# Performance work log

Measured on AMD Instinct MI355X. Metric: run time of the kernel, lower is better.

Reference implementation:

```python
import jax, jax.numpy as jnp
import numpy as np

H = 256   # hidden_dim
S = 16    # d_state
B = 2
N = 8192
LN_EPS = 1e-5


def setup_inputs() -> dict:
    key = jax.random.key(0)
    ks = jax.random.split(key, 12)
    std = 1.0 / np.sqrt(H)
    inp = {
        'x': jax.random.normal(ks[0], (B, N, H), dtype=jnp.float32),
        'in_w': jax.random.normal(ks[1], (2 * H, H), dtype=jnp.float32) * std,
        'in_b': jax.random.normal(ks[2], (2 * H,), dtype=jnp.float32) * std,
        'xp_w': jax.random.normal(ks[3], (2 * S + 1, H), dtype=jnp.float32) * std,
        'xp_b': jax.random.normal(ks[4], (2 * S + 1,), dtype=jnp.float32) * std,
        'dt_w': jax.random.normal(ks[5], (H, 1), dtype=jnp.float32),
        'dt_b': jax.random.normal(ks[6], (H,), dtype=jnp.float32),
        'A_log': jnp.log(jnp.broadcast_to(jnp.arange(1, S + 1, dtype=jnp.float32), (H, S))),
        'D': jnp.ones((H,), dtype=jnp.float32),
        'out_w': jax.random.normal(ks[7], (H, H), dtype=jnp.float32) * std,
        'out_b': jax.random.normal(ks[8], (H,), dtype=jnp.float32) * std,
        'ln_g': jnp.ones((H,), dtype=jnp.float32),
        'ln_b': jnp.zeros((H,), dtype=jnp.float32),
    }
    return inp


def reference(x, in_w, in_b, xp_w, xp_b, dt_w, dt_b, A_log, D, out_w, out_b, ln_g, ln_b):
    # x: (B, N, H). Dropout is identity in eval mode.
    residual = x
    xz = jnp.einsum('bnh,kh->bnk', x, in_w) + in_b            # (B,N,2H)
    x_inner, z = xz[..., :H], xz[..., H:]
    x_dbl = jnp.einsum('bnh,kh->bnk', x_inner, xp_w) + xp_b   # (B,N,2S+1)
    dt_raw = x_dbl[..., :1]
    B_raw = x_dbl[..., 1:S + 1]                               # (B,N,S)
    C_raw = x_dbl[..., S + 1:]                                # (B,N,S)
    dt = jax.nn.softplus(dt_raw * dt_w[:, 0] + dt_b)          # (B,N,H)
    # NOTE: the original computes dA = exp(dt * A) but never uses it; A_log
    # does not affect the output, so we skip materializing dA.
    dB = dt[..., None] * B_raw[:, :, None, :]                 # (B,N,H,S)
    h = jnp.cumsum(x_inner[..., None] * dB, axis=1)           # (B,N,H,S)
    y = jnp.einsum('bnhs,bns->bnh', h, C_raw) + D * x_inner   # (B,N,H)
    y = y * jax.nn.silu(z)
    out = jnp.einsum('bnh,kh->bnk', y, out_w) + out_b
    r = out + residual
    mu = jnp.mean(r, axis=-1, keepdims=True)
    var = jnp.mean((r - mu) ** 2, axis=-1, keepdims=True)
    return ln_g * (r - mu) * jax.lax.rsqrt(var + LN_EPS) + ln_b
```

## Files before the change

kernel.cpp:

```cpp
#include <hip/hip_runtime.h>
#include <hip/hip_bf16.h>


#define HD 256
#define SD 16
#define NSEQ 8192
#define NBATCH 2
#define BN (NBATCH * NSEQ)
#define CHUNK 32
#define NCHUNK (NSEQ / CHUNK)
#define NGRP 16
#define GSZ (NCHUNK / NGRP)
#define LN_EPS 1e-5f
#define UST 40
#define YST 257

#define NX  (BN * HD)
#define NIW (2 * HD * HD)
#define NXP (48 * HD)
#define NOW (HD * HD)

typedef __hip_bfloat16 bf16;
typedef __attribute__((ext_vector_type(8))) short bf16x8;
typedef __attribute__((ext_vector_type(4))) short short4v;
typedef __attribute__((ext_vector_type(4))) float f32x4;
typedef __attribute__((ext_vector_type(4))) unsigned int uint4v;
typedef __attribute__((ext_vector_type(2))) unsigned int uint2v;

__device__ __forceinline__ float b2f(bf16 v) { return __bfloat162float(v); }
__device__ __forceinline__ short f2bs(float f) {
  union { bf16 b; short s; } u;
  u.b = __float2bfloat16(f);
  return u.s;
}
__device__ __forceinline__ unsigned int pack2(float a, float b) {
  return (unsigned int)(unsigned short)f2bs(a) |
         ((unsigned int)(unsigned short)f2bs(b) << 16);
}
__device__ __forceinline__ bf16x8 cvt_frag(const float* p) {
  bf16x8 r;
#pragma unroll
  for (int j = 0; j < 8; ++j) r[j] = f2bs(p[j]);
  return r;
}
__device__ __forceinline__ float softplus_f(float a) {
  return (a > 20.f) ? a : __logf(1.f + __expf(a));
}

__global__ __launch_bounds__(256) void k0_convert(
    const float* __restrict__ x, const float* __restrict__ in_w,
    const float* __restrict__ xp_w, const float* __restrict__ out_w,
    bf16* __restrict__ xb, bf16* __restrict__ wbin,
    bf16* __restrict__ wbxp, bf16* __restrict__ wbout)
{
  const int base = (blockIdx.x * 256 + threadIdx.x) * 4;
  if (base < NX) {
    f32x4 v = *(const f32x4*)(x + base);
    *(short4v*)((short*)xb + base) =
        short4v{f2bs(v[0]), f2bs(v[1]), f2bs(v[2]), f2bs(v[3])};
  } else if (base < NX + NIW) {
    const int off = base - NX;
    f32x4 v = *(const f32x4*)(in_w + off);
    *(short4v*)((short*)wbin + off) =
        short4v{f2bs(v[0]), f2bs(v[1]), f2bs(v[2]), f2bs(v[3])};
  } else if (base < NX + NIW + NXP) {
    const int off = base - NX - NIW;
    short4v s;
    if (off < 33 * HD) {
      f32x4 v = *(const f32x4*)(xp_w + off);
      s = short4v{f2bs(v[0]), f2bs(v[1]), f2bs(v[2]), f2bs(v[3])};
    } else {
      s = short4v{0, 0, 0, 0};
    }
    *(short4v*)((short*)wbxp + off) = s;
  } else if (base < NX + NIW + NXP + NOW) {
    const int off = base - NX - NIW - NXP;
    f32x4 v = *(const f32x4*)(out_w + off);
    *(short4v*)((short*)wbout + off) =
        short4v{f2bs(v[0]), f2bs(v[1]), f2bs(v[2]), f2bs(v[3])};
  }
}

__global__ __launch_bounds__(256) void k1_gemm(
    const bf16* __restrict__ xb, const bf16* __restrict__ wbin,
    const float* __restrict__ in_b, bf16* __restrict__ xib,
    bf16* __restrict__ zb)
{
  __shared__ __align__(16) char smem[128 * 264 * 2];
  bf16* Bt = (bf16*)smem;
  float* Ct = (float*)smem;

  const int tid = threadIdx.x;
  const int rt = blockIdx.x >> 2, ct = blockIdx.x & 3;
  const int R0 = rt * 128, C0 = ct * 128;
  const int wave = tid >> 6, lane = tid & 63, q = lane >> 4, l16 = lane & 15;

#pragma unroll
  for (int it = 0; it < 16; ++it) {
    const int f = tid + it * 256;
    const int row = f >> 5, g = f & 31;
    bf16x8 v = *(const bf16x8*)(wbin + (size_t)(C0 + row) * HD + g * 8);
    *(bf16x8*)(Bt + row * 264 + g * 8) = v;
  }
  __syncthreads();

  const int rowHalf = (wave & 1) * 64;
  const int colHalf = (wave >> 1) * 64;
  f32x4 acc[4][4] = {};
  const bf16* ap = xb + (size_t)(R0 + rowHalf + l16) * HD + q * 8;
#pragma unroll
  for (int k = 0; k < HD; k += 32) {
    bf16x8 a[4], b[4];
#pragma unroll
    for (int i = 0; i < 4; ++i)
      a[i] = *(const bf16x8*)(ap + (size_t)i * 16 * HD + k);
#pragma unroll
    for (int j = 0; j < 4; ++j)
      b[j] = *(const bf16x8*)(Bt + (colHalf + j * 16 + l16) * 264 + k + q * 8);
#pragma unroll
    for (int i = 0; i < 4; ++i)
#pragma unroll
      for (int j = 0; j < 4; ++j)
        acc[i][j] = __builtin_amdgcn_mfma_f32_16x16x32_bf16(a[i], b[j], acc[i][j], 0, 0, 0);
  }
  __syncthreads();

#pragma unroll
  for (int j = 0; j < 4; ++j) {
    const int col = colHalf + j * 16 + l16;
    const float bias = in_b[C0 + col];
#pragma unroll
    for (int i = 0; i < 4; ++i)
#pragma unroll
      for (int r = 0; r < 4; ++r)
        Ct[(rowHalf + i * 16 + q * 4 + r) * 132 + col] = acc[i][j][r] + bias;
  }
  __syncthreads();

  bf16* dst = (C0 < HD) ? xib : zb;
  const int Cd = (C0 < HD) ? C0 : (C0 - HD);
#pragma unroll
  for (int it = 0; it < 8; ++it) {
    const int f = tid + it * 256;
    const int row = f >> 4, g = f & 15;
    bf16x8 v = cvt_frag(Ct + row * 132 + g * 8);
    *(bf16x8*)(dst + (size_t)(R0 + row) * HD + Cd + g * 8) = v;
  }
}

__global__ __launch_bounds__(256) void kS_xp_sum(
    const bf16* __restrict__ xib, const bf16* __restrict__ wbxp,
    const float* __restrict__ xp_b, const float* __restrict__ dt_w,
    const float* __restrict__ dt_b, float* __restrict__ dbc,
    bf16* __restrict__ Tg, float* __restrict__ Mc)
{
  __shared__ __align__(16) bf16 xt[32 * 264];
  __shared__ __align__(16) bf16 wp[48 * 264];
  __shared__ __align__(16) float sdbc[32][33];
  __shared__ __align__(16) bf16 sBt[16 * UST];
  __shared__ __align__(16) bf16 Ut[256 * UST];
  const int tid = threadIdx.x;
  const int wave = tid >> 6, lane = tid & 63, q = lane >> 4, l16 = lane & 15;
  const int cix = blockIdx.x;
  const int R0 = cix * CHUNK;

#pragma unroll
  for (int it = 0; it < 4; ++it) {
    const int f = tid + it * 256, row = f >> 5, g = f & 31;
    *(bf16x8*)(xt + row * 264 + g * 8) =
        *(const bf16x8*)(xib + (size_t)(R0 + row) * HD + g * 8);
  }
#pragma unroll
  for (int it = 0; it < 6; ++it) {
    const int f = tid + it * 256, row = f >> 5, g = f & 31;
    *(bf16x8*)(wp + row * 264 + g * 8) =
        *(const bf16x8*)(wbxp + (size_t)row * HD + g * 8);
  }
  __syncthreads();

  if (wave < 2) {
    f32x4 pacc[3] = {};
#pragma unroll
    for (int k = 0; k < HD; k += 32) {
      bf16x8 af = *(const bf16x8*)(xt + (wave * 16 + l16) * 264 + k + q * 8);
#pragma unroll
      for (int t = 0; t < 3; ++t) {
        bf16x8 bfr = *(const bf16x8*)(wp + (t * 16 + l16) * 264 + k + q * 8);
        pacc[t] = __builtin_amdgcn_mfma_f32_16x16x32_bf16(af, bfr, pacc[t], 0, 0, 0);
      }
    }
#pragma unroll
    for (int t = 0; t < 3; ++t) {
      const int col = t * 16 + l16;
      if (col < 33) {
        const float bias = xp_b[col];
#pragma unroll
        for (int r = 0; r < 4; ++r) {
          const int row = wave * 16 + q * 4 + r;
          const float v = pacc[t][r] + bias;
          sdbc[row][col] = v;
          if (col >= 1 && col < 17)
            *((short*)sBt + (col - 1) * UST + row) = f2bs(v);
        }
      }
    }
  }
  __syncthreads();

  {
    const float* sflat = &sdbc[0][0];
    for (int idx = tid; idx < CHUNK * 33; idx += 256)
      dbc[(size_t)R0 * 33 + idx] = sflat[idx];
  }
  {
    const int h = tid;
    const float dtw = dt_w[h], dtb = dt_b[h];
    unsigned int up[16];
#pragma unroll
    for (int n2 = 0; n2 < 16; ++n2) {
      const int n = 2 * n2;
      const float xv0 = b2f(xt[n * 264 + h]);
      const float xv1 = b2f(xt[(n + 1) * 264 + h]);
      const float u0 = xv0 * softplus_f(sdbc[n][0] * dtw + dtb);
      const float u1 = xv1 * softplus_f(sdbc[n + 1][0] * dtw + dtb);
      up[n2] = pack2(u0, u1);
    }
    uint4v* dst = (uint4v*)(Ut + h * UST);
#pragma unroll
    for (int j = 0; j < 4; ++j)
      dst[j] = uint4v{up[4 * j], up[4 * j + 1], up[4 * j + 2], up[4 * j + 3]};
  }
  {
    const int n = tid >> 3;
    const int m0 = (tid & 7) * 4;
    float cn[SD];
#pragma unroll
    for (int s = 0; s < SD; ++s) cn[s] = sdbc[n][17 + s];
    short4v tv;
#pragma unroll
    for (int mm = 0; mm < 4; ++mm) {
      const int m = m0 + mm;
      float t = 0.f;
#pragma unroll
      for (int s = 0; s < SD; ++s) t += cn[s] * sdbc[m][1 + s];
      tv[mm] = (m <= n) ? f2bs(t) : (short)0;
    }
    *(short4v*)((short*)Tg + (size_t)cix * 1024 + n * 32 + m0) = tv;
  }
  __syncthreads();

  {
    bf16x8 af = *(const bf16x8*)(sBt + l16 * UST + q * 8);
    f32x4 macc[4] = {};
#pragma unroll
    for (int c4 = 0; c4 < 4; ++c4) {
      const int ct = wave * 4 + c4;
      bf16x8 bu = *(const bf16x8*)(Ut + (ct * 16 + l16) * UST + q * 8);
      macc[c4] = __builtin_amdgcn_mfma_f32_16x16x32_bf16(af, bu, macc[c4], 0, 0, 0);
    }
    float* mbase = Mc + (size_t)cix * 4096;
#pragma unroll
    for (int c4 = 0; c4 < 4; ++c4) {
      const int h = (wave * 4 + c4) * 16 + l16;
#pragma unroll
      for (int r = 0; r < 4; ++r)
        mbase[(q * 4 + r) * HD + h] = macc[c4][r];
    }
  }
}

__global__ __launch_bounds__(256) void k4a_prefix_local(
    float* __restrict__ Mc, float* __restrict__ Gs)
{
  const int tid = blockIdx.x * 256 + threadIdx.x;
  const int b = tid >> 16;
  const int g = (tid >> 12) & (NGRP - 1);
  const int hs = tid & 4095;
  float run = 0.f;
#pragma unroll
  for (int i = 0; i < GSZ; ++i) {
    const size_t idx = ((size_t)(b * NCHUNK + g * GSZ + i)) * 4096 + hs;
    const float v = Mc[idx];
    Mc[idx] = run;
    run += v;
  }
  Gs[((size_t)(b * NGRP + g)) * 4096 + hs] = run;
}

__global__ __launch_bounds__(256) void k4b_prefix_groups(float* __restrict__ Gs)
{
  const int tid = blockIdx.x * 256 + threadIdx.x;
  const int b = tid >> 12;
  const int hs = tid & 4095;
  float run = 0.f;
#pragma unroll
  for (int g = 0; g < NGRP; ++g) {
    const size_t idx = ((size_t)(b * NGRP + g)) * 4096 + hs;
    const float v = Gs[idx];
    Gs[idx] = run;
    run += v;
  }
}

__global__ __launch_bounds__(256) void k56_scan_out_ln(
    const bf16* __restrict__ xib, const bf16* __restrict__ zb,
    const float* __restrict__ dbc, const bf16* __restrict__ Tg,
    const float* __restrict__ dt_w, const float* __restrict__ dt_b,
    const float* __restrict__ Dv, const float* __restrict__ Mc,
    const float* __restrict__ Gs, const bf16* __restrict__ wbout,
    const float* __restrict__ out_b, const float* __restrict__ x,
    const float* __restrict__ ln_g, const float* __restrict__ ln_b,
    float* __restrict__ out)
{
  __shared__ __align__(16) char un[2 * 32 * YST * 4];
  bf16* Ut  = (bf16*)un;
  bf16* Hst = (bf16*)(un + 20480);
  bf16* Ctl = (bf16*)(un + 40960);
  bf16* Tt  = (bf16*)(un + 43520);
  float* yt = (float*)un;
  float* pt = (float*)(un + 32 * YST * 4);
  __shared__ float sdt[32];

  const int tid = threadIdx.x;
  const int wave = tid >> 6, lane = tid & 63, q = lane >> 4, l16 = lane & 15;
  const int cix = blockIdx.x;
  const int R0 = cix * CHUNK;
  const int b = cix >> 8;
  const int cchunk = cix & 255;

  *(short4v*)((short*)Tt + tid * 4) =
      *(const short4v*)((const short*)Tg + (size_t)cix * 1024 + tid * 4);
  if (tid < 32) sdt[tid] = dbc[(size_t)(R0 + tid) * 33];
  {
    const int n = tid >> 3, k0 = (tid & 7) * 4;
    float v[4];
#pragma unroll
    for (int j = 0; j < 4; ++j) {
      const int k = k0 + j;
      v[j] = (k < SD) ? dbc[(size_t)(R0 + n) * 33 + 17 + k] : 0.f;
    }
    *(uint2v*)((short*)Ctl + n * UST + k0) = uint2v{pack2(v[0], v[1]), pack2(v[2], v[3])};
  }
  {
    const int h = tid;
    const float* mp = Mc + (size_t)cix * 4096 + h;
    const float* gp = Gs + ((size_t)(b * NGRP + cchunk / GSZ)) * 4096 + h;
    unsigned int hp[8];
#pragma unroll
    for (int s2 = 0; s2 < 8; ++s2) {
      const int s = 2 * s2;
      const float v0 = mp[s * HD] + gp[s * HD];
      const float v1 = mp[(s + 1) * HD] + gp[(s + 1) * HD];
      hp[s2] = pack2(v0, v1);
    }
    uint4v* hd = (uint4v*)(Hst + h * UST);
    hd[0] = uint4v{hp[0], hp[1], hp[2], hp[3]};
    hd[1] = uint4v{hp[4], hp[5], hp[6], hp[7]};
    hd[2] = uint4v{0, 0, 0, 0};
    hd[3] = uint4v{0, 0, 0, 0};
  }
  __syncthreads();

  {
    const int h = tid;
    const float dtw = dt_w[h], dtb = dt_b[h];
    unsigned int up[16];
#pragma unroll
    for (int n2 = 0; n2 < 16; ++n2) {
      const int n = 2 * n2;
      const float xv0 = b2f(xib[(size_t)(R0 + n) * HD + h]);
      const float xv1 = b2f(xib[(size_t)(R0 + n + 1) * HD + h]);
      const float u0 = xv0 * softplus_f(sdt[n] * dtw + dtb);
      const float u1 = xv1 * softplus_f(sdt[n + 1] * dtw + dtb);
      up[n2] = pack2(u0, u1);
    }
    uint4v* dst = (uint4v*)(Ut + h * UST);
#pragma unroll
    for (int j = 0; j < 4; ++j)
      dst[j] = uint4v{up[4 * j], up[4 * j + 1], up[4 * j + 2], up[4 * j + 3]};
  }
  __syncthreads();

  f32x4 acc[2][4] = {};
  {
    bf16x8 aT0 = *(const bf16x8*)(Tt + l16 * 32 + q * 8);
    bf16x8 aT1 = *(const bf16x8*)(Tt + (16 + l16) * 32 + q * 8);
    bf16x8 aC0 = *(const bf16x8*)(Ctl + l16 * UST + q * 8);
    bf16x8 aC1 = *(const bf16x8*)(Ctl + (16 + l16) * UST + q * 8);
#pragma unroll
    for (int c4 = 0; c4 < 4; ++c4) {
      const int ct = wave * 4 + c4;
      bf16x8 bu = *(const bf16x8*)(Ut + (ct * 16 + l16) * UST + q * 8);
      bf16x8 bh = *(const bf16x8*)(Hst + (ct * 16 + l16) * UST + q * 8);
      acc[0][c4] = __builtin_amdgcn_mfma_f32_16x16x32_bf16(aT0, bu, acc[0][c4], 0, 0, 0);
      acc[0][c4] = __builtin_amdgcn_mfma_f32_16x16x32_bf16(aC0, bh, acc[0][c4], 0, 0, 0);
      acc[1][c4] = __builtin_amdgcn_mfma_f32_16x16x32_bf16(aT1, bu, acc[1][c4], 0, 0, 0);
      acc[1][c4] = __builtin_amdgcn_mfma_f32_16x16x32_bf16(aC1, bh, acc[1][c4], 0, 0, 0);
    }
  }
  __syncthreads();

#pragma unroll
  for (int c4 = 0; c4 < 4; ++c4) {
    const int h = (wave * 4 + c4) * 16 + l16;
#pragma unroll
    for (int rt = 0; rt < 2; ++rt)
#pragma unroll
      for (int r = 0; r < 4; ++r)
        yt[(rt * 16 + q * 4 + r) * YST + h] = acc[rt][c4][r];
  }
  __syncthreads();

  {
    const int h = tid;
    const float dh = Dv[h];
#pragma unroll
    for (int n = 0; n < CHUNK; ++n) {
      const size_t row = (size_t)(R0 + n) * HD + h;
      const float yv = yt[n * YST + h] + dh * b2f(xib[row]);
      const float zv = b2f(zb[row]);
      const float sig = 1.f / (1.f + __expf(-zv));
      yt[n * YST + h] = yv * zv * sig;
    }
  }
  __syncthreads();

  const int cw = wave * 64;
  f32x4 oacc[2][4] = {};
#pragma unroll
  for (int k = 0; k < HD; k += 32) {
    bf16x8 a0 = cvt_frag(&yt[l16 * YST + k + q * 8]);
    bf16x8 a1 = cvt_frag(&yt[(16 + l16) * YST + k + q * 8]);
#pragma unroll
    for (int t = 0; t < 4; ++t) {
      bf16x8 bfr = *(const bf16x8*)(wbout + (size_t)(cw + t * 16 + l16) * HD + k + q * 8);
      oacc[0][t] = __builtin_amdgcn_mfma_f32_16x16x32_bf16(a0, bfr, oacc[0][t], 0, 0, 0);
      oacc[1][t] = __builtin_amdgcn_mfma_f32_16x16x32_bf16(a1, bfr, oacc[1][t], 0, 0, 0);
    }
  }
#pragma unroll
  for (int t = 0; t < 4; ++t) {
    const int col = cw + t * 16 + l16;
    const float bias = out_b[col];
#pragma unroll
    for (int rt = 0; rt < 2; ++rt)
#pragma unroll
      for (int r = 0; r < 4; ++r) {
        const int row = rt * 16 + q * 4 + r;
        pt[row * YST + col] = oacc[rt][t][r] + bias + x[(size_t)(R0 + row) * HD + col];
      }
  }
  __syncthreads();

#pragma unroll
  for (int rr = 0; rr < 8; ++rr) {
    const int row = wave * 8 + rr;
    float p = 0.f;
#pragma unroll
    for (int j = 0; j < 4; ++j) p += pt[row * YST + lane + 64 * j];
#pragma unroll
    for (int off = 32; off > 0; off >>= 1) p += __shfl_xor(p, off);
    const float mu = p * (1.f / 256.f);
    float v2 = 0.f;
#pragma unroll
    for (int j = 0; j < 4; ++j) {
      const float d = pt[row * YST + lane + 64 * j] - mu;
      v2 += d * d;
    }
#pragma unroll
    for (int off = 32; off > 0; off >>= 1) v2 += __shfl_xor(v2, off);
    const float rstd = rsqrtf(v2 * (1.f / 256.f) + LN_EPS);
    const size_t base = (size_t)(R0 + row) * HD;
#pragma unroll
    for (int j = 0; j < 4; ++j) {
      const int cc = lane + 64 * j;
      out[base + cc] = ln_g[cc] * (pt[row * YST + cc] - mu) * rstd + ln_b[cc];
    }
  }
}

extern "C" void kernel_launch(void* const* d_in, const int* in_sizes, int n_in,
                              void* d_out, int out_size, void* d_ws, size_t ws_size,
                              hipStream_t stream)
{
  const float* x     = (const float*)d_in[0];
  const float* in_w  = (const float*)d_in[1];
  const float* in_b  = (const float*)d_in[2];
  const float* xp_w  = (const float*)d_in[3];
  const float* xp_b  = (const float*)d_in[4];
  const float* dt_w  = (const float*)d_in[5];
  const float* dt_b  = (const float*)d_in[6];
  const float* Dv    = (const float*)d_in[8];
  const float* out_w = (const float*)d_in[9];
  const float* out_b = (const float*)d_in[10];
  const float* ln_g  = (const float*)d_in[11];
  const float* ln_b  = (const float*)d_in[12];

  char* ws = (char*)d_ws;
  bf16*  xib   = (bf16*)(ws);
  bf16*  zb    = (bf16*)(ws +  8388608);
  bf16*  xb    = (bf16*)(ws + 16777216);
  float* dbc   = (float*)(ws + 25165824);
  float* Mc    = (float*)(ws + 27328512);
  float* Gs    = (float*)(ws + 35717120);
  bf16*  wbin  = (bf16*)(ws + 36241408);
  bf16*  wbxp  = (bf16*)(ws + 36503552);
  bf16*  wbout = (bf16*)(ws + 36528128);
  bf16*  Tg    = (bf16*)(ws + 36659200);
  float* out   = (float*)d_out;

  hipLaunchKernelGGL(k0_convert, dim3((NX + NIW + NXP + NOW) / 1024), dim3(256),
                     0, stream, x, in_w, xp_w, out_w, xb, wbin, wbxp, wbout);
  hipLaunchKernelGGL(k1_gemm, dim3(512), dim3(256), 0, stream,
                     xb, wbin, in_b, xib, zb);
  hipLaunchKernelGGL(kS_xp_sum, dim3(BN / CHUNK), dim3(256), 0, stream,
                     xib, wbxp, xp_b, dt_w, dt_b, dbc, Tg, Mc);
  hipLaunchKernelGGL(k4a_prefix_local, dim3(NBATCH * NGRP * 4096 / 256),
                     dim3(256), 0, stream, Mc, Gs);
  hipLaunchKernelGGL(k4b_prefix_groups, dim3(NBATCH * 4096 / 256), dim3(256),
                     0, stream, Gs);
  hipLaunchKernelGGL(k56_scan_out_ln, dim3(BN / CHUNK), dim3(256), 0, stream,
                     xib, zb, dbc, Tg, dt_w, dt_b, Dv, Mc, Gs,
                     wbout, out_b, x, ln_g, ln_b, out);
}
```

Before: 144.0 us.

## Recompute intra-chunk C·B matrix in scan kernel and stage y as bf16

Moves the per-chunk lower-triangular C·B (T) matrix computation from the xp kernel into the scan/output kernel, removing the Tg global write and read. The dbc chunk is staged in shared memory once and reused. The y epilogue (D skip, SiLU gate) is fused directly into the MFMA accumulator registers and written as bf16 into LDS, eliminating an fp32 staging pass and a barrier and shrinking LDS. Cost is extra ALU work in the scan kernel and a different LDS aliasing layout.

```diff
diff --git a/kernel.cpp b/kernel.cpp
--- a/kernel.cpp
+++ b/kernel.cpp
@@ -13,7 +13,7 @@
 #define GSZ (NCHUNK / NGRP)
 #define LN_EPS 1e-5f
 #define UST 40
-#define YST 257
+#define PST 257
 
 #define NX  (BN * HD)
 #define NIW (2 * HD * HD)
@@ -152,7 +152,7 @@
     const bf16* __restrict__ xib, const bf16* __restrict__ wbxp,
     const float* __restrict__ xp_b, const float* __restrict__ dt_w,
     const float* __restrict__ dt_b, float* __restrict__ dbc,
-    bf16* __restrict__ Tg, float* __restrict__ Mc)
+    float* __restrict__ Mc)
 {
   __shared__ __align__(16) bf16 xt[32 * 264];
   __shared__ __align__(16) bf16 wp[48 * 264];
@@ -230,23 +230,6 @@
     for (int j = 0; j < 4; ++j)
       dst[j] = uint4v{up[4 * j], up[4 * j + 1], up[4 * j + 2], up[4 * j + 3]};
   }
-  {
-    const int n = tid >> 3;
-    const int m0 = (tid & 7) * 4;
-    float cn[SD];
-#pragma unroll
-    for (int s = 0; s < SD; ++s) cn[s] = sdbc[n][17 + s];
-    short4v tv;
-#pragma unroll
-    for (int mm = 0; mm < 4; ++mm) {
-      const int m = m0 + mm;
-      float t = 0.f;
-#pragma unroll
-      for (int s = 0; s < SD; ++s) t += cn[s] * sdbc[m][1 + s];
-      tv[mm] = (m <= n) ? f2bs(t) : (short)0;
-    }
-    *(short4v*)((short*)Tg + (size_t)cix * 1024 + n * 32 + m0) = tv;
-  }
   __syncthreads();
 
   {
@@ -304,22 +287,21 @@
 
 __global__ __launch_bounds__(256) void k56_scan_out_ln(
     const bf16* __restrict__ xib, const bf16* __restrict__ zb,
-    const float* __restrict__ dbc, const bf16* __restrict__ Tg,
-    const float* __restrict__ dt_w, const float* __restrict__ dt_b,
-    const float* __restrict__ Dv, const float* __restrict__ Mc,
-    const float* __restrict__ Gs, const bf16* __restrict__ wbout,
-    const float* __restrict__ out_b, const float* __restrict__ x,
-    const float* __restrict__ ln_g, const float* __restrict__ ln_b,
-    float* __restrict__ out)
-{
-  __shared__ __align__(16) char un[2 * 32 * YST * 4];
+    const float* __restrict__ dbc, const float* __restrict__ dt_w,
+    const float* __restrict__ dt_b, const float* __restrict__ Dv,
+    const float* __restrict__ Mc, const float* __restrict__ Gs,
+    const bf16* __restrict__ wbout, const float* __restrict__ out_b,
+    const float* __restrict__ x, const float* __restrict__ ln_g,
+    const float* __restrict__ ln_b, float* __restrict__ out)
+{
+  __shared__ __align__(16) char un[53376];
   bf16* Ut  = (bf16*)un;
   bf16* Hst = (bf16*)(un + 20480);
   bf16* Ctl = (bf16*)(un + 40960);
   bf16* Tt  = (bf16*)(un + 43520);
-  float* yt = (float*)un;
-  float* pt = (float*)(un + 32 * YST * 4);
-  __shared__ float sdt[32];
+  bf16* yb  = (bf16*)un;
+  float* pt = (float*)(un + 20480);
+  __shared__ float sdbc[32][33];
 
   const int tid = threadIdx.x;
   const int wave = tid >> 6, lane = tid & 63, q = lane >> 4, l16 = lane & 15;
@@ -328,16 +310,37 @@
   const int b = cix >> 8;
   const int cchunk = cix & 255;
 
-  *(short4v*)((short*)Tt + tid * 4) =
-      *(const short4v*)((const short*)Tg + (size_t)cix * 1024 + tid * 4);
-  if (tid < 32) sdt[tid] = dbc[(size_t)(R0 + tid) * 33];
+  {
+    float* sflat = &sdbc[0][0];
+    for (int idx = tid; idx < CHUNK * 33; idx += 256)
+      sflat[idx] = dbc[(size_t)R0 * 33 + idx];
+  }
+  __syncthreads();
+
+  {
+    const int n = tid >> 3;
+    const int m0 = (tid & 7) * 4;
+    float cn[SD];
+#pragma unroll
+    for (int s = 0; s < SD; ++s) cn[s] = sdbc[n][17 + s];
+    short4v tv;
+#pragma unroll
+    for (int mm = 0; mm < 4; ++mm) {
+      const int m = m0 + mm;
+      float t = 0.f;
+#pragma unroll
+      for (int s = 0; s < SD; ++s) t += cn[s] * sdbc[m][1 + s];
+      tv[mm] = (m <= n) ? f2bs(t) : (short)0;
+    }
+    *(short4v*)((short*)Tt + n * 32 + m0) = tv;
+  }
   {
     const int n = tid >> 3, k0 = (tid & 7) * 4;
     float v[4];
 #pragma unroll
     for (int j = 0; j < 4; ++j) {
       const int k = k0 + j;
-      v[j] = (k < SD) ? dbc[(size_t)(R0 + n) * 33 + 17 + k] : 0.f;
+      v[j] = (k < SD) ? sdbc[n][17 + k] : 0.f;
     }
     *(uint2v*)((short*)Ctl + n * UST + k0) = uint2v{pack2(v[0], v[1]), pack2(v[2], v[3])};
   }
@@ -359,8 +362,6 @@
     hd[2] = uint4v{0, 0, 0, 0};
     hd[3] = uint4v{0, 0, 0, 0};
   }
-  __syncthreads();
-
   {
     const int h = tid;
     const float dtw = dt_w[h], dtb = dt_b[h];
@@ -370,8 +371,8 @@
       const int n = 2 * n2;
       const float xv0 = b2f(xib[(size_t)(R0 + n) * HD + h]);
       const float xv1 = b2f(xib[(size_t)(R0 + n + 1) * HD + h]);
-      const float u0 = xv0 * softplus_f(sdt[n] * dtw + dtb);
-      const float u1 = xv1 * softplus_f(sdt[n + 1] * dtw + dtb);
+      const float u0 = xv0 * softplus_f(sdbc[n][0] * dtw + dtb);
+      const float u1 = xv1 * softplus_f(sdbc[n + 1][0] * dtw + dtb);
       up[n2] = pack2(u0, u1);
     }
     uint4v* dst = (uint4v*)(Ut + h * UST);
@@ -400,27 +401,23 @@
   }
   __syncthreads();
 
-#pragma unroll
-  for (int c4 = 0; c4 < 4; ++c4) {
-    const int h = (wave * 4 + c4) * 16 + l16;
-#pragma unroll
-    for (int rt = 0; rt < 2; ++rt)
-#pragma unroll
-      for (int r = 0; r < 4; ++r)
-        yt[(rt * 16 + q * 4 + r) * YST + h] = acc[rt][c4][r];
-  }
-  __syncthreads();
-
-  {
-    const int h = tid;
-    const float dh = Dv[h];
-#pragma unroll
-    for (int n = 0; n < CHUNK; ++n) {
-      const size_t row = (size_t)(R0 + n) * HD + h;
-      const float yv = yt[n * YST + h] + dh * b2f(xib[row]);
-      const float zv = b2f(zb[row]);
-      const float sig = 1.f / (1.f + __expf(-zv));
-      yt[n * YST + h] = yv * zv * sig;
+  {
+#pragma unroll
+    for (int c4 = 0; c4 < 4; ++c4) {
+      const int h = (wave * 4 + c4) * 16 + l16;
+      const float dh = Dv[h];
+#pragma unroll
+      for (int rt = 0; rt < 2; ++rt)
+#pragma unroll
+        for (int r = 0; r < 4; ++r) {
+          const int n = rt * 16 + q * 4 + r;
+          const size_t grow = (size_t)(R0 + n) * HD + h;
+          const float xv = b2f(xib[grow]);
+          const float zv = b2f(zb[grow]);
+          const float yv = acc[rt][c4][r] + dh * xv;
+          const float sig = 1.f / (1.f + __expf(-zv));
+          ((short*)yb)[n * 264 + h] = f2bs(yv * zv * sig);
+        }
     }
   }
   __syncthreads();
@@ -429,8 +426,8 @@
   f32x4 oacc[2][4] = {};
 #pragma unroll
   for (int k = 0; k < HD; k += 32) {
-    bf16x8 a0 = cvt_frag(&yt[l16 * YST + k + q * 8]);
-    bf16x8 a1 = cvt_frag(&yt[(16 + l16) * YST + k + q * 8]);
+    bf16x8 a0 = *(const bf16x8*)(yb + l16 * 264 + k + q * 8);
+    bf16x8 a1 = *(const bf16x8*)(yb + (16 + l16) * 264 + k + q * 8);
 #pragma unroll
     for (int t = 0; t < 4; ++t) {
       bf16x8 bfr = *(const bf16x8*)(wbout + (size_t)(cw + t * 16 + l16) * HD + k + q * 8);
@@ -447,7 +444,7 @@
 #pragma unroll
       for (int r = 0; r < 4; ++r) {
         const int row = rt * 16 + q * 4 + r;
-        pt[row * YST + col] = oacc[rt][t][r] + bias + x[(size_t)(R0 + row) * HD + col];
+        pt[row * PST + col] = oacc[rt][t][r] + bias + x[(size_t)(R0 + row) * HD + col];
       }
   }
   __syncthreads();
@@ -457,14 +454,14 @@
     const int row = wave * 8 + rr;
     float p = 0.f;
 #pragma unroll
-    for (int j = 0; j < 4; ++j) p += pt[row * YST + lane + 64 * j];
+    for (int j = 0; j < 4; ++j) p += pt[row * PST + lane + 64 * j];
 #pragma unroll
     for (int off = 32; off > 0; off >>= 1) p += __shfl_xor(p, off);
     const float mu = p * (1.f / 256.f);
     float v2 = 0.f;
 #pragma unroll
     for (int j = 0; j < 4; ++j) {
-      const float d = pt[row * YST + lane + 64 * j] - mu;
+      const float d = pt[row * PST + lane + 64 * j] - mu;
       v2 += d * d;
     }
 #pragma unroll
@@ -474,7 +471,7 @@
 #pragma unroll
     for (int j = 0; j < 4; ++j) {
       const int cc = lane + 64 * j;
-      out[base + cc] = ln_g[cc] * (pt[row * YST + cc] - mu) * rstd + ln_b[cc];
+      out[base + cc] = ln_g[cc] * (pt[row * PST + cc] - mu) * rstd + ln_b[cc];
     }
   }
 }
@@ -506,7 +503,6 @@
   bf16*  wbin  = (bf16*)(ws + 36241408);
   bf16*  wbxp  = (bf16*)(ws + 36503552);
   bf16*  wbout = (bf16*)(ws + 36528128);
-  bf16*  Tg    = (bf16*)(ws + 36659200);
   float* out   = (float*)d_out;
 
   hipLaunchKernelGGL(k0_convert, dim3((NX + NIW + NXP + NOW) / 1024), dim3(256),
@@ -514,12 +510,12 @@
   hipLaunchKernelGGL(k1_gemm, dim3(512), dim3(256), 0, stream,
                      xb, wbin, in_b, xib, zb);
   hipLaunchKernelGGL(kS_xp_sum, dim3(BN / CHUNK), dim3(256), 0, stream,
-                     xib, wbxp, xp_b, dt_w, dt_b, dbc, Tg, Mc);
+                     xib, wbxp, xp_b, dt_w, dt_b, dbc, Mc);
   hipLaunchKernelGGL(k4a_prefix_local, dim3(NBATCH * NGRP * 4096 / 256),
                      dim3(256), 0, stream, Mc, Gs);
   hipLaunchKernelGGL(k4b_prefix_groups, dim3(NBATCH * 4096 / 256), dim3(256),
                      0, stream, Gs);
   hipLaunchKernelGGL(k56_scan_out_ln, dim3(BN / CHUNK), dim3(256), 0, stream,
-                     xib, zb, dbc, Tg, dt_w, dt_b, Dv, Mc, Gs,
+                     xib, zb, dbc, dt_w, dt_b, Dv, Mc, Gs,
                      wbout, out_b, x, ln_g, ln_b, out);
 }
```

New measurement: 143.2 us. No clear change (-0.5%).
